# Kernel tuning notes

Hardware: AMD Instinct MI355X
Metric: run time of the kernel (lower is better)

The kernel has to match this reference:

```python
import jax, jax.numpy as jnp
import numpy as np
import math

B, N, CS, CZ = 2, 512, 384, 128
H, C, PQ, PV = 12, 16, 4, 8
EPS = 1e-8

def _quat_to_rot(q):
    q = q / jnp.linalg.norm(q, axis=-1, keepdims=True)
    a, b, c, d = q[..., 0], q[..., 1], q[..., 2], q[..., 3]
    return jnp.stack([
        jnp.stack([a*a+b*b-c*c-d*d, 2*(b*c-a*d), 2*(b*d+a*c)], -1),
        jnp.stack([2*(b*c+a*d), a*a-b*b+c*c-d*d, 2*(c*d-a*b)], -1),
        jnp.stack([2*(b*d-a*c), 2*(c*d+a*b), a*a-b*b-c*c+d*d], -1)], -2)

def setup_inputs() -> dict:
    key = jax.random.key(0)
    ks = jax.random.split(key, 12)
    def lin(k, out_f, in_f):
        return jax.random.normal(k, (out_f, in_f), jnp.float32) * math.sqrt(1.0 / in_f)
    inp = {}
    inp['single'] = jax.random.normal(ks[0], (B, N, CS), jnp.float32)
    inp['pair'] = jax.random.normal(ks[1], (B, N, N, CZ), jnp.float32)
    inp['rotations'] = _quat_to_rot(jax.random.normal(ks[2], (B, N, 4), jnp.float32))
    inp['translations'] = jax.random.normal(ks[3], (B, N, 3), jnp.float32) * 10.0
    inp['wq'] = lin(ks[4], H*C, CS); inp['bq'] = jnp.zeros((H*C,), jnp.float32)
    inp['wkv'] = lin(ks[5], 2*H*C, CS); inp['bkv'] = jnp.zeros((2*H*C,), jnp.float32)
    inp['wqp'] = lin(ks[6], 3*H*PQ, CS); inp['bqp'] = jnp.zeros((3*H*PQ,), jnp.float32)
    inp['wkvp'] = lin(ks[7], 3*H*(PQ+PV), CS); inp['bkvp'] = jnp.zeros((3*H*(PQ+PV),), jnp.float32)
    inp['wb'] = lin(ks[8], H, CZ); inp['bb'] = jnp.zeros((H,), jnp.float32)
    out_in = H*C + H*PV*4 + H*CZ  # scalar + (x,y,z,norm) points + pair
    inp['wo'] = lin(ks[9], CS, out_in); inp['bo'] = jnp.zeros((CS,), jnp.float32)
    inp['head_weights'] = jax.random.normal(ks[10], (H,), jnp.float32) * 0.1
    return inp

def _ipa(single, pair, rotations, translations, wq, bq, wkv, bkv, wqp, bqp, wkvp, bkvp, wb, bb, wo, bo, head_weights):
    b_, n_ = single.shape[0], single.shape[1]
    # scalar q/k/v
    q = (single @ wq.T + bq).reshape(b_, n_, H, C)
    kv = (single @ wkv.T + bkv).reshape(b_, n_, H, 2*C)
    k, v = kv[..., :C], kv[..., C:]
    # point q/k/v in local frames (chunk into x,y,z then stack, per _project_points)
    def proj_pts(w, bvec, P):
        raw = single @ w.T + bvec
        xc, yc, zc = jnp.split(raw, 3, axis=-1)
        return jnp.stack([xc, yc, zc], -1).reshape(b_, n_, H, P, 3)
    q_pts = proj_pts(wqp, bqp, PQ)
    kv_pts = proj_pts(wkvp, bkvp, PQ + PV)
    k_pts, v_pts = kv_pts[..., :PQ, :], kv_pts[..., PQ:, :]
    # apply rigid frames: global = R @ p + t
    def to_global(p):
        return jnp.einsum('biop,bihqp->bihqo', rotations, p) + translations[:, :, None, None, :]
    qg, kg, vg = to_global(q_pts), to_global(k_pts), to_global(v_pts)
    # scalar logits + pair bias
    bias = pair @ wb.T + bb  # [B,N,N,H]
    logits = jnp.einsum('bihc,bjhc->bhij', q, k) * math.sqrt(1.0 / (3.0 * C))
    logits = logits + math.sqrt(1.0 / 3.0) * bias.transpose(0, 3, 1, 2)
    # point-distance logits
    d2 = jnp.sum((qg[:, :, None] - kg[:, None]) ** 2, axis=-1)  # [B,N,N,H,PQ]
    gamma = jax.nn.softplus(head_weights)  # [H]
    wpt = math.sqrt(1.0 / (3.0 * PQ * 4.5))
    pt_logits = -0.5 * wpt * jnp.sum(d2, axis=-1) * gamma  # [B,N,N,H]
    attn = jax.nn.softmax(logits + pt_logits.transpose(0, 3, 1, 2), axis=-1)  # [B,H,N,N]
    # assemble output features
    out_scalar = jnp.einsum('bhij,bjhc->bihc', attn, v).reshape(b_, n_, H*C)
    rp_g = jnp.einsum('bhij,bjhpc->bihpc', attn, vg)
    # back to local frame: R^T @ (p - t)
    rp_l = jnp.einsum('bipo,bihqp->bihqo', rotations, rp_g - translations[:, :, None, None, :])
    norms = jnp.sqrt(jnp.sum(rp_l ** 2, -1) + EPS).reshape(b_, n_, H*PV)
    rp_l = rp_l.reshape(b_, n_, H*PV, 3)
    out_pair = jnp.einsum('bhij,bijd->bihd', attn, pair).reshape(b_, n_, H*CZ)
    feats = jnp.concatenate([out_scalar, rp_l[..., 0], rp_l[..., 1], rp_l[..., 2], norms, out_pair], -1)
    return feats @ wo.T + bo

def reference(single, pair, rotations, translations, wq, bq, wkv, bkv, wqp, bqp, wkvp, bkvp, wb, bb, wo, bo, head_weights):
    return _ipa(single, pair, rotations, translations, wq, bq, wkv, bkv, wqp, bqp, wkvp, bkvp, wb, bb, wo, bo, head_weights)
```

## Files before the change

### kernel.cpp

```cpp
#include <hip/hip_runtime.h>
#include <hip/hip_bf16.h>
#include <math.h>

#define NB 2
#define NN 512
#define CSD 384
#define CZD 128
#define NH 12
#define NC 16
#define NPQ 4
#define NPV 8
#define HC 192
#define QPDIM 144
#define FEATD 2112
#define WPT 0.13608276348795434f
#define RS3C 0.14433756729740643f
#define RS3 0.5773502691896258f

typedef __attribute__((ext_vector_type(8))) short short8;
typedef __attribute__((ext_vector_type(4))) float f32x4;

static __device__ inline unsigned short f2bf(float x) {
    __hip_bfloat16 h = __float2bfloat16(x);
    return *reinterpret_cast<unsigned short*>(&h);
}
static __device__ inline unsigned short bflo(float x) {
    __hip_bfloat16 h = __float2bfloat16(x);
    return f2bf(x - __bfloat162float(h));
}

#define R_S0 393216
#define R_S1 (R_S0 + 73728)
#define R_S2 (R_S1 + 147456)
#define R_S3 (R_S2 + 55296)
#define R_S4 (R_S3 + 165888)
#define R_S5 (R_S4 + 811008)
#define R_S6 (R_S5 + 2048)
__global__ __launch_bounds__(256) void k_cvt(
    const float* __restrict__ single, const float* __restrict__ wq,
    const float* __restrict__ wkv, const float* __restrict__ wqp,
    const float* __restrict__ wkvp, const float* __restrict__ wo,
    const float* __restrict__ wb,
    unsigned short* __restrict__ singleb, unsigned short* __restrict__ wallb,
    unsigned short* __restrict__ wob, unsigned short* __restrict__ wbb)
{
    int gid = blockIdx.x * 256 + threadIdx.x;
    int e = gid * 4;
    if (e >= R_S6) return;
    if (e >= R_S5) {
        int c = e - R_S5;
        int hh = c >> 7;
        ushort4 o;
        if (hh < 12) {
            float4 v = *(const float4*)(wb + hh * 128 + (c & 127));
            o.x = f2bf(v.x); o.y = f2bf(v.y); o.z = f2bf(v.z); o.w = f2bf(v.w);
        } else { o.x = 0; o.y = 0; o.z = 0; o.w = 0; }
        *(ushort4*)(wbb + c) = o;
        return;
    }
    const float* src; unsigned short* dst;
    if (e < R_S0)      { src = single + e;          dst = singleb + e; }
    else if (e < R_S1) { src = wq + (e - R_S0);     dst = wallb + (e - R_S0); }
    else if (e < R_S2) { src = wkv + (e - R_S1);    dst = wallb + 73728 + (e - R_S1); }
    else if (e < R_S3) { src = wqp + (e - R_S2);    dst = wallb + 221184 + (e - R_S2); }
    else if (e < R_S4) { src = wkvp + (e - R_S3);   dst = wallb + 276480 + (e - R_S3); }
    else               { src = wo + (e - R_S4);     dst = wob + (e - R_S4); }
    float4 v = *(const float4*)src;
    ushort4 o;
    o.x = f2bf(v.x); o.y = f2bf(v.y); o.z = f2bf(v.z); o.w = f2bf(v.w);
    *(ushort4*)dst = o;
}

__global__ __launch_bounds__(256) void k_gemm1(
    const unsigned short* __restrict__ A, const unsigned short* __restrict__ Bm,
    float* __restrict__ Cr)
{
    int w = threadIdx.x >> 6, lane = threadIdx.x & 63;
    int rt = blockIdx.x;
    int ct = blockIdx.y * 4 + w;
    int r = lane & 15, kq = lane >> 4;
    const unsigned short* ap = A  + (size_t)(rt * 16 + r) * 384 + kq * 8;
    const unsigned short* bp = Bm + (size_t)(ct * 16 + r) * 384 + kq * 8;
    f32x4 acc = {0.f, 0.f, 0.f, 0.f};
    #pragma unroll 4
    for (int ks = 0; ks < 12; ++ks) {
        short8 av = *(const short8*)(ap + ks * 32);
        short8 bv = *(const short8*)(bp + ks * 32);
        acc = __builtin_amdgcn_mfma_f32_16x16x32_bf16(av, bv, acc, 0, 0, 0);
    }
    int crow = rt * 16 + kq * 4;
    int ccol = ct * 16 + r;
    #pragma unroll
    for (int i = 0; i < 4; ++i)
        Cr[(size_t)(crow + i) * 1152 + ccol] = acc[i];
}

__global__ __launch_bounds__(256) void k_post(
    const float* __restrict__ praw, const float* __restrict__ rot, const float* __restrict__ trans,
    const float* __restrict__ hw,
    const float* __restrict__ bq, const float* __restrict__ bkv,
    const float* __restrict__ bqp, const float* __restrict__ bkvp,
    unsigned short* __restrict__ vallT2,
    unsigned short* __restrict__ qhat, unsigned short* __restrict__ khat,
    float* __restrict__ qn2, float* __restrict__ kn2)
{
    __shared__ float s_q[192], s_k[192], s_v[192], s_qp[QPDIM], s_kvp[432];
    __shared__ float s_qg[144], s_kg[144], s_vg[288];
    __shared__ float s_sh[12];
    const int t = threadIdx.x;
    const int row = blockIdx.x;
    const int b = row >> 9;
    const int i = row & 511;

    if (t < 12) {
        float sp = log1pf(expf(hw[t]));
        s_sh[t] = RS3C / (WPT * sp);
    }
    const float* pr = praw + (size_t)row * 1152;
    for (int idx = t; idx < 1152; idx += 256) {
        float v = pr[idx];
        if (idx < 192) {
            s_q[idx] = v + bq[idx];
        } else if (idx < 576) {
            int f = idx - 192; float x = v + bkv[f];
            int h = f >> 5, cc = f & 31;
            if (cc < 16) s_k[h * 16 + cc] = x;
            else         s_v[h * 16 + cc - 16] = x;
        } else if (idx < 720) {
            int f = idx - 576; s_qp[f] = v + bqp[f];
        } else {
            int f = idx - 720; s_kvp[f] = v + bkvp[f];
        }
    }
    __syncthreads();

    if (t < 192) {
        const float* R = rot + (size_t)row * 9;
        const float* T = trans + (size_t)row * 3;
        float lx, ly, lz; float* dst;
        if (t < 48) {
            lx = s_qp[t]; ly = s_qp[48 + t]; lz = s_qp[96 + t];
            dst = s_qg + t * 3;
        } else if (t < 96) {
            int idx = t - 48; int fb = (idx >> 2) * 12 + (idx & 3);
            lx = s_kvp[fb]; ly = s_kvp[144 + fb]; lz = s_kvp[288 + fb];
            dst = s_kg + idx * 3;
        } else {
            int idx = t - 96; int fb = (idx >> 3) * 12 + 4 + (idx & 7);
            lx = s_kvp[fb]; ly = s_kvp[144 + fb]; lz = s_kvp[288 + fb];
            dst = s_vg + idx * 3;
        }
        dst[0] = R[0] * lx + R[1] * ly + R[2] * lz + T[0];
        dst[1] = R[3] * lx + R[4] * ly + R[5] * lz + T[1];
        dst[2] = R[6] * lx + R[7] * ly + R[8] * lz + T[2];
    }
    __syncthreads();

    if (t < 24) {
        int h = t % 12;
        const float* g = (t < 12) ? (s_qg + h * 12) : (s_kg + h * 12);
        float s = 0.f;
        #pragma unroll
        for (int e = 0; e < 12; ++e) s += g[e] * g[e];
        float* dst = (t < 12) ? qn2 : kn2;
        dst[((size_t)b * 12 + h) * 512 + i] = s;
    }

    for (int c = t; c < 768; c += 256) {
        int h = c >> 6, cp = c & 63;
        unsigned short v;
        if (cp < 16)      v = f2bf(s_v[h * 16 + cp]);
        else if (cp < 40) v = f2bf(s_vg[h * 24 + cp - 16]);
        else              v = bflo(s_vg[h * 24 + cp - 40]);
        vallT2[((size_t)(b * 12 + h) * 64 + cp) * 512 + i] = v;
    }

    for (int idx = t; idx < 768; idx += 256) {
        int side = idx >= 384;
        int li = side ? (idx - 384) : idx;
        int h = li >> 5, s2 = li & 31;
        unsigned short o[2];
        #pragma unroll
        for (int u = 0; u < 2; ++u) {
            int k = 2 * s2 + u;
            unsigned short val = 0;
            if (!side) {
                if (k < 16)      val = f2bf(s_sh[h] * s_q[h * 16 + k]);
                else if (k < 28) val = f2bf(s_qg[h * 12 + k - 16]);
                else if (k < 40) val = f2bf(s_qg[h * 12 + k - 28]);
                else if (k < 52) val = bflo(s_qg[h * 12 + k - 40]);
            } else {
                if (k < 16)      val = f2bf(s_k[h * 16 + k]);
                else if (k < 28) val = f2bf(s_kg[h * 12 + k - 16]);
                else if (k < 40) val = bflo(s_kg[h * 12 + k - 28]);
                else if (k < 52) val = f2bf(s_kg[h * 12 + k - 40]);
            }
            o[u] = val;
        }
        unsigned short* dst = (side ? khat : qhat) + (((size_t)b * 12 + h) * 512 + i) * 64 + 2 * s2;
        *(ushort2*)dst = make_ushort2(o[0], o[1]);
    }
}

__global__ __launch_bounds__(256) void k_qk(
    const unsigned short* __restrict__ qhat, const unsigned short* __restrict__ khat,
    const float* __restrict__ qn2, const float* __restrict__ kn2,
    const float* __restrict__ hw, float* __restrict__ plog)
{
    int w = threadIdx.x >> 6, lane = threadIdx.x & 63;
    int bh = blockIdx.x;
    int i0 = (blockIdx.y >> 3) * 64;
    int j0 = (blockIdx.y & 7) * 64;
    int r = lane & 15, kq = lane >> 4;
    float sp = log1pf(expf(hw[bh % 12]));
    float m = WPT * sp;
    float coef = -0.5f * m;

    const unsigned short* ap = qhat + ((size_t)bh * 512 + i0 + w * 16 + r) * 64 + kq * 8;
    short8 a0 = *(const short8*)(ap);
    short8 a1 = *(const short8*)(ap + 32);
    const unsigned short* bpb = khat + ((size_t)bh * 512 + j0 + r) * 64 + kq * 8;
    f32x4 acc[4];
    #pragma unroll
    for (int jt = 0; jt < 4; ++jt) {
        short8 b0 = *(const short8*)(bpb + (size_t)jt * 1024);
        short8 b1 = *(const short8*)(bpb + (size_t)jt * 1024 + 32);
        f32x4 a = {0.f, 0.f, 0.f, 0.f};
        a = __builtin_amdgcn_mfma_f32_16x16x32_bf16(a0, b0, a, 0, 0, 0);
        a = __builtin_amdgcn_mfma_f32_16x16x32_bf16(a1, b1, a, 0, 0, 0);
        acc[jt] = a;
    }
    int crow = i0 + w * 16 + kq * 4;
    const float* qn = qn2 + (size_t)bh * 512;
    const float* kn = kn2 + (size_t)bh * 512;
    #pragma unroll
    for (int jt = 0; jt < 4; ++jt) {
        int ccol = j0 + jt * 16 + r;
        float knv = kn[ccol];
        #pragma unroll
        for (int ii = 0; ii < 4; ++ii)
            plog[((size_t)bh * 512 + crow + ii) * 512 + ccol] =
                m * acc[jt][ii] + coef * (qn[crow + ii] + knv);
    }
}

__global__ __launch_bounds__(512) void k_av(
    const float* __restrict__ pair,
    const unsigned short* __restrict__ wbb, const float* __restrict__ bb,
    const float* __restrict__ plog,
    unsigned short* __restrict__ attnb, unsigned short* __restrict__ featsb)
{
    __shared__ float attn12[12][521];

    const int t = threadIdx.x;
    const int row_i = blockIdx.x;
    const int b = row_i >> 9;
    const int i_loc = row_i & 511;
    const int w = t >> 6, lane = t & 63;
    const int r = lane & 15, kq = lane >> 4;

    {
        const unsigned short* bp = wbb + r * 128 + kq * 8;
        short8 bfrag[4];
        #pragma unroll
        for (int ks = 0; ks < 4; ++ks) bfrag[ks] = *(const short8*)(bp + ks * 32);
        float bbv = (r < 12) ? bb[r] : 0.f;
        #pragma unroll
        for (int tt = 0; tt < 4; ++tt) {
            int tile = w + tt * 8;
            const float* ap = pair + ((size_t)row_i * NN + tile * 16 + r) * CZD + kq * 8;
            float4 p[8];
            #pragma unroll
            for (int ks = 0; ks < 4; ++ks) {
                p[2 * ks]     = *(const float4*)(ap + ks * 32);
                p[2 * ks + 1] = *(const float4*)(ap + ks * 32 + 4);
            }
            f32x4 acc = {0.f, 0.f, 0.f, 0.f};
            #pragma unroll
            for (int ks = 0; ks < 4; ++ks) {
                short8 av;
                av[0] = (short)f2bf(p[2*ks].x);   av[1] = (short)f2bf(p[2*ks].y);
                av[2] = (short)f2bf(p[2*ks].z);   av[3] = (short)f2bf(p[2*ks].w);
                av[4] = (short)f2bf(p[2*ks+1].x); av[5] = (short)f2bf(p[2*ks+1].y);
                av[6] = (short)f2bf(p[2*ks+1].z); av[7] = (short)f2bf(p[2*ks+1].w);
                acc = __builtin_amdgcn_mfma_f32_16x16x32_bf16(av, bfrag[ks], acc, 0, 0, 0);
            }
            if (r < 12) {
                #pragma unroll
                for (int ii = 0; ii < 4; ++ii)
                    attn12[r][tile * 16 + kq * 4 + ii] = RS3 * (acc[ii] + bbv);
            }
        }
    }
    __syncthreads();

    #pragma unroll
    for (int it = 0; it < 3; ++it) {
        int idx4 = it * 512 + t;
        int h = idx4 >> 7;
        int j4 = (idx4 & 127) * 4;
        const float* lp = plog + (((size_t)b * 12 + h) * 512 + i_loc) * 512 + j4;
        float4 lv = *(const float4*)lp;
        attn12[h][j4 + 0] += lv.x;
        attn12[h][j4 + 1] += lv.y;
        attn12[h][j4 + 2] += lv.z;
        attn12[h][j4 + 3] += lv.w;
    }
    __syncthreads();

    for (int hh = w; hh < 12; hh += 8) {
        float vreg[8];
        float mx = -1e30f;
        #pragma unroll
        for (int s = 0; s < 8; ++s) { vreg[s] = attn12[hh][lane + 64 * s]; mx = fmaxf(mx, vreg[s]); }
        #pragma unroll
        for (int off = 32; off >= 1; off >>= 1) mx = fmaxf(mx, __shfl_xor(mx, off, 64));
        float ssum = 0.f;
        #pragma unroll
        for (int s = 0; s < 8; ++s) { vreg[s] = __expf(vreg[s] - mx); ssum += vreg[s]; }
        #pragma unroll
        for (int off = 32; off >= 1; off >>= 1) ssum += __shfl_xor(ssum, off, 64);
        float inv = 1.0f / ssum;
        #pragma unroll
        for (int s = 0; s < 8; ++s) attn12[hh][lane + 64 * s] = vreg[s] * inv;
    }
    __syncthreads();

    for (int idx = t; idx < 768; idx += 512) {
        int h = idx >> 6, jc = idx & 63;
        ushort4 o0, o1;
        o0.x = f2bf(attn12[h][jc * 8 + 0]); o0.y = f2bf(attn12[h][jc * 8 + 1]);
        o0.z = f2bf(attn12[h][jc * 8 + 2]); o0.w = f2bf(attn12[h][jc * 8 + 3]);
        o1.x = f2bf(attn12[h][jc * 8 + 4]); o1.y = f2bf(attn12[h][jc * 8 + 5]);
        o1.z = f2bf(attn12[h][jc * 8 + 6]); o1.w = f2bf(attn12[h][jc * 8 + 7]);
        unsigned short* gp = attnb + (((size_t)(b * 12 + h) * 512 + i_loc)) * 512 + jc * 8;
        *(ushort4*)gp = o0;
        *(ushort4*)(gp + 4) = o1;
    }
    __syncthreads();

    {
        const int d0 = w * 16;
        const int hr = (r < 12) ? r : 11;
        const unsigned short* arow = attnb + (((size_t)(b * 12 + hr) * 512 + i_loc)) * 512 + kq * 8;
        const float* pbase = pair + (size_t)row_i * NN * CZD + d0 + r;
        f32x4 acc = {0.f, 0.f, 0.f, 0.f};
        for (int ks = 0; ks < 16; ++ks) {
            int jb = ks * 32 + kq * 8;
            float x0 = pbase[(size_t)(jb + 0) * CZD];
            float x1 = pbase[(size_t)(jb + 1) * CZD];
            float x2 = pbase[(size_t)(jb + 2) * CZD];
            float x3 = pbase[(size_t)(jb + 3) * CZD];
            float x4 = pbase[(size_t)(jb + 4) * CZD];
            float x5 = pbase[(size_t)(jb + 5) * CZD];
            float x6 = pbase[(size_t)(jb + 6) * CZD];
            float x7 = pbase[(size_t)(jb + 7) * CZD];
            short8 av = *(const short8*)(arow + ks * 32);
            short8 bv;
            bv[0] = (short)f2bf(x0); bv[1] = (short)f2bf(x1);
            bv[2] = (short)f2bf(x2); bv[3] = (short)f2bf(x3);
            bv[4] = (short)f2bf(x4); bv[5] = (short)f2bf(x5);
            bv[6] = (short)f2bf(x6); bv[7] = (short)f2bf(x7);
            acc = __builtin_amdgcn_mfma_f32_16x16x32_bf16(av, bv, acc, 0, 0, 0);
        }
        unsigned short* frow = featsb + (size_t)row_i * FEATD;
        if (kq < 3) {
            #pragma unroll
            for (int ii = 0; ii < 4; ++ii)
                frow[576 + (kq * 4 + ii) * CZD + d0 + r] = f2bf(acc[ii]);
        }
    }
}

__global__ __launch_bounds__(512) void k_avg(
    const unsigned short* __restrict__ attnb, const unsigned short* __restrict__ vallT2,
    float* __restrict__ rpg, unsigned short* __restrict__ featsb)
{
    int bh = blockIdx.x;
    int itile = blockIdx.y;
    int b = bh / 12, h = bh % 12;
    int w = threadIdx.x >> 6, lane = threadIdx.x & 63;
    int mt = w >> 2, nt = w & 3;
    int r = lane & 15, kq = lane >> 4;
    int i0 = itile * 32 + mt * 16;
    const unsigned short* ap = attnb + ((size_t)bh * 512 + i0 + r) * 512 + kq * 8;
    const unsigned short* bp = vallT2 + ((size_t)bh * 64 + nt * 16 + r) * 512 + kq * 8;
    f32x4 acc = {0.f, 0.f, 0.f, 0.f};
    #pragma unroll
    for (int ks = 0; ks < 16; ++ks) {
        short8 av = *(const short8*)(ap + ks * 32);
        short8 bv = *(const short8*)(bp + ks * 32);
        acc = __builtin_amdgcn_mfma_f32_16x16x32_bf16(av, bv, acc, 0, 0, 0);
    }
    int cp = nt * 16 + r;
    #pragma unroll
    for (int ii = 0; ii < 4; ++ii) {
        int i = i0 + kq * 4 + ii;
        size_t rowg = (size_t)b * 512 + i;
        if (nt == 0) {
            featsb[rowg * FEATD + h * 16 + r] = f2bf(acc[ii]);
        } else {
            rpg[rowg * 576 + h * 48 + (cp - 16)] = acc[ii];
        }
    }
}

__global__ __launch_bounds__(128) void k_rp(
    const float* __restrict__ rpg, const float* __restrict__ rot, const float* __restrict__ trans,
    unsigned short* __restrict__ featsb)
{
    __shared__ float rot_s[9], trans_s[3];
    int row = blockIdx.x, t = threadIdx.x;
    if (t < 9) rot_s[t] = rot[(size_t)row * 9 + t];
    if (t >= 9 && t < 12) trans_s[t - 9] = trans[(size_t)row * 3 + (t - 9)];
    __syncthreads();
    if (t < 96) {
        int h = t >> 3, p = t & 7;
        const float* rp = rpg + (size_t)row * 576 + h * 48;
        float g0 = rp[p * 3 + 0] + rp[24 + p * 3 + 0];
        float g1 = rp[p * 3 + 1] + rp[24 + p * 3 + 1];
        float g2 = rp[p * 3 + 2] + rp[24 + p * 3 + 2];
        float d0 = g0 - trans_s[0], d1 = g1 - trans_s[1], d2v = g2 - trans_s[2];
        float l0 = rot_s[0] * d0 + rot_s[3] * d1 + rot_s[6] * d2v;
        float l1 = rot_s[1] * d0 + rot_s[4] * d1 + rot_s[7] * d2v;
        float l2 = rot_s[2] * d0 + rot_s[5] * d1 + rot_s[8] * d2v;
        float nrm = sqrtf(l0 * l0 + l1 * l1 + l2 * l2 + 1e-8f);
        unsigned short* frow = featsb + (size_t)row * FEATD;
        int hp = h * 8 + p;
        frow[192 + hp] = f2bf(l0);
        frow[288 + hp] = f2bf(l1);
        frow[384 + hp] = f2bf(l2);
        frow[480 + hp] = f2bf(nrm);
    }
}

__global__ __launch_bounds__(256) void k_gemm2(
    const unsigned short* __restrict__ A, const unsigned short* __restrict__ Bm,
    const float* __restrict__ bo, float* __restrict__ out)
{
    int w = threadIdx.x >> 6, lane = threadIdx.x & 63;
    int rt = blockIdx.x;
    int ct = blockIdx.y * 4 + w;
    int r = lane & 15, kq = lane >> 4;
    const unsigned short* ap = A  + (size_t)(rt * 16 + r) * FEATD + kq * 8;
    const unsigned short* bp = Bm + (size_t)(ct * 16 + r) * FEATD + kq * 8;
    f32x4 acc = {0.f, 0.f, 0.f, 0.f};
    #pragma unroll 2
    for (int ks = 0; ks < 66; ++ks) {
        short8 av = *(const short8*)(ap + ks * 32);
        short8 bv = *(const short8*)(bp + ks * 32);
        acc = __builtin_amdgcn_mfma_f32_16x16x32_bf16(av, bv, acc, 0, 0, 0);
    }
    int crow = rt * 16 + kq * 4;
    int ccol = ct * 16 + r;
    float bv = bo[ccol];
    #pragma unroll
    for (int i = 0; i < 4; ++i)
        out[(size_t)(crow + i) * CSD + ccol] = acc[i] + bv;
}

extern "C" void kernel_launch(void* const* d_in, const int* in_sizes, int n_in,
                              void* d_out, int out_size, void* d_ws, size_t ws_size,
                              hipStream_t stream) {
    const float* single = (const float*)d_in[0];
    const float* pair   = (const float*)d_in[1];
    const float* rot    = (const float*)d_in[2];
    const float* trans  = (const float*)d_in[3];
    const float* wq     = (const float*)d_in[4];
    const float* bq     = (const float*)d_in[5];
    const float* wkv    = (const float*)d_in[6];
    const float* bkv    = (const float*)d_in[7];
    const float* wqp    = (const float*)d_in[8];
    const float* bqp    = (const float*)d_in[9];
    const float* wkvp   = (const float*)d_in[10];
    const float* bkvp   = (const float*)d_in[11];
    const float* wb     = (const float*)d_in[12];
    const float* bb     = (const float*)d_in[13];
    const float* wo     = (const float*)d_in[14];
    const float* bo     = (const float*)d_in[15];
    const float* hw     = (const float*)d_in[16];
    float* out = (float*)d_out;

    float* ws = (float*)d_ws;
    float* plog    = ws;
    float* projraw = ws;
    unsigned short* qhat = (unsigned short*)(ws + 6291456);
    unsigned short* khat = (unsigned short*)(ws + 6684672);
    float* qn2     = ws + 7077888;
    float* kn2     = ws + 7090176;
    unsigned short* featsb  = (unsigned short*)(ws + 7102464);
    unsigned short* singleb = (unsigned short*)(ws + 8183808);
    unsigned short* wallb   = (unsigned short*)(ws + 8380416);
    unsigned short* wob     = (unsigned short*)(ws + 8601600);
    unsigned short* wbb     = (unsigned short*)(ws + 9007104);
    unsigned short* vallT2  = (unsigned short*)(ws + 9008128);
    unsigned short* attnb   = (unsigned short*)(ws + 9401344);
    float* rpg     = ws + 12547072;

    hipLaunchKernelGGL(k_cvt, dim3(1610), dim3(256), 0, stream,
                       single, wq, wkv, wqp, wkvp, wo, wb, singleb, wallb, wob, wbb);
    hipLaunchKernelGGL(k_gemm1, dim3(64, 18), dim3(256), 0, stream, singleb, wallb, projraw);
    hipLaunchKernelGGL(k_post, dim3(1024), dim3(256), 0, stream,
                       projraw, rot, trans, hw, bq, bkv, bqp, bkvp,
                       vallT2, qhat, khat, qn2, kn2);
    hipLaunchKernelGGL(k_qk, dim3(24, 64), dim3(256), 0, stream,
                       qhat, khat, qn2, kn2, hw, plog);
    hipLaunchKernelGGL(k_av, dim3(1024), dim3(512), 0, stream,
                       pair, wbb, bb, plog, attnb, featsb);
    hipLaunchKernelGGL(k_avg, dim3(24, 16), dim3(512), 0, stream,
                       attnb, vallT2, rpg, featsb);
    hipLaunchKernelGGL(k_rp, dim3(1024), dim3(128), 0, stream, rpg, rot, trans, featsb);
    hipLaunchKernelGGL(k_gemm2, dim3(64, 6), dim3(256), 0, stream, featsb, wob, bo, out);
}
```

Baseline: 187.6 us.

## Stage pair tiles through LDS transpose in k_av and fuse point transform into k_avg

```diff
diff --git a/kernel.cpp b/kernel.cpp
--- a/kernel.cpp
+++ b/kernel.cpp
@@ -250,7 +250,9 @@
     const float* __restrict__ plog,
     unsigned short* __restrict__ attnb, unsigned short* __restrict__ featsb)
 {
-    __shared__ float attn12[12][521];
+    __shared__ __align__(16) unsigned char smem_raw[34816];
+    float (*attn12)[521] = (float(*)[521])smem_raw;
+    unsigned short* ldsT = (unsigned short*)smem_raw;
 
     const int t = threadIdx.x;
     const int row_i = blockIdx.x;
@@ -343,43 +345,53 @@
         const int d0 = w * 16;
         const int hr = (r < 12) ? r : 11;
         const unsigned short* arow = attnb + (((size_t)(b * 12 + hr) * 512 + i_loc)) * 512 + kq * 8;
-        const float* pbase = pair + (size_t)row_i * NN * CZD + d0 + r;
+        const int jl = t >> 2, dq = t & 3;
+        const float* srcb = pair + (size_t)row_i * NN * CZD + dq * 32;
         f32x4 acc = {0.f, 0.f, 0.f, 0.f};
-        for (int ks = 0; ks < 16; ++ks) {
-            int jb = ks * 32 + kq * 8;
-            float x0 = pbase[(size_t)(jb + 0) * CZD];
-            float x1 = pbase[(size_t)(jb + 1) * CZD];
-            float x2 = pbase[(size_t)(jb + 2) * CZD];
-            float x3 = pbase[(size_t)(jb + 3) * CZD];
-            float x4 = pbase[(size_t)(jb + 4) * CZD];
-            float x5 = pbase[(size_t)(jb + 5) * CZD];
-            float x6 = pbase[(size_t)(jb + 6) * CZD];
-            float x7 = pbase[(size_t)(jb + 7) * CZD];
-            short8 av = *(const short8*)(arow + ks * 32);
-            short8 bv;
-            bv[0] = (short)f2bf(x0); bv[1] = (short)f2bf(x1);
-            bv[2] = (short)f2bf(x2); bv[3] = (short)f2bf(x3);
-            bv[4] = (short)f2bf(x4); bv[5] = (short)f2bf(x5);
-            bv[6] = (short)f2bf(x6); bv[7] = (short)f2bf(x7);
-            acc = __builtin_amdgcn_mfma_f32_16x16x32_bf16(av, bv, acc, 0, 0, 0);
+        for (int st = 0; st < 4; ++st) {
+            const float* src = srcb + (size_t)(st * 128 + jl) * CZD;
+            float4 vv[8];
+            #pragma unroll
+            for (int u = 0; u < 8; ++u) vv[u] = *(const float4*)(src + u * 4);
+            #pragma unroll
+            for (int u = 0; u < 8; ++u) {
+                int d = dq * 32 + u * 4;
+                ldsT[(size_t)(d + 0) * 136 + jl] = f2bf(vv[u].x);
+                ldsT[(size_t)(d + 1) * 136 + jl] = f2bf(vv[u].y);
+                ldsT[(size_t)(d + 2) * 136 + jl] = f2bf(vv[u].z);
+                ldsT[(size_t)(d + 3) * 136 + jl] = f2bf(vv[u].w);
+            }
+            __syncthreads();
+            #pragma unroll
+            for (int ks = 0; ks < 4; ++ks) {
+                short8 av = *(const short8*)(arow + st * 128 + ks * 32);
+                short8 bv = *(const short8*)(ldsT + (size_t)(d0 + r) * 136 + ks * 32 + kq * 8);
+                acc = __builtin_amdgcn_mfma_f32_16x16x32_bf16(av, bv, acc, 0, 0, 0);
+            }
+            __syncthreads();
         }
         unsigned short* frow = featsb + (size_t)row_i * FEATD;
         if (kq < 3) {
             #pragma unroll
-            for (int ii = 0; ii < 4; ++ii)
-                frow[576 + (kq * 4 + ii) * CZD + d0 + r] = f2bf(acc[ii]);
+            for (int ii = 0; ii < 4; ++ii) {
+                int h = kq * 4 + ii;
+                frow[576 + h * CZD + d0 + r] = f2bf(acc[ii]);
+            }
         }
     }
 }
 
 __global__ __launch_bounds__(512) void k_avg(
     const unsigned short* __restrict__ attnb, const unsigned short* __restrict__ vallT2,
-    float* __restrict__ rpg, unsigned short* __restrict__ featsb)
-{
+    const float* __restrict__ rot, const float* __restrict__ trans,
+    unsigned short* __restrict__ featsb)
+{
+    __shared__ float rp_s[32][49];
     int bh = blockIdx.x;
     int itile = blockIdx.y;
     int b = bh / 12, h = bh % 12;
-    int w = threadIdx.x >> 6, lane = threadIdx.x & 63;
+    int t = threadIdx.x;
+    int w = t >> 6, lane = t & 63;
     int mt = w >> 2, nt = w & 3;
     int r = lane & 15, kq = lane >> 4;
     int i0 = itile * 32 + mt * 16;
@@ -395,37 +407,29 @@
     int cp = nt * 16 + r;
     #pragma unroll
     for (int ii = 0; ii < 4; ++ii) {
-        int i = i0 + kq * 4 + ii;
-        size_t rowg = (size_t)b * 512 + i;
+        int il = mt * 16 + kq * 4 + ii;
         if (nt == 0) {
+            size_t rowg = (size_t)b * 512 + itile * 32 + il;
             featsb[rowg * FEATD + h * 16 + r] = f2bf(acc[ii]);
         } else {
-            rpg[rowg * 576 + h * 48 + (cp - 16)] = acc[ii];
-        }
-    }
-}
-
-__global__ __launch_bounds__(128) void k_rp(
-    const float* __restrict__ rpg, const float* __restrict__ rot, const float* __restrict__ trans,
-    unsigned short* __restrict__ featsb)
-{
-    __shared__ float rot_s[9], trans_s[3];
-    int row = blockIdx.x, t = threadIdx.x;
-    if (t < 9) rot_s[t] = rot[(size_t)row * 9 + t];
-    if (t >= 9 && t < 12) trans_s[t - 9] = trans[(size_t)row * 3 + (t - 9)];
-    __syncthreads();
-    if (t < 96) {
-        int h = t >> 3, p = t & 7;
-        const float* rp = rpg + (size_t)row * 576 + h * 48;
-        float g0 = rp[p * 3 + 0] + rp[24 + p * 3 + 0];
-        float g1 = rp[p * 3 + 1] + rp[24 + p * 3 + 1];
-        float g2 = rp[p * 3 + 2] + rp[24 + p * 3 + 2];
-        float d0 = g0 - trans_s[0], d1 = g1 - trans_s[1], d2v = g2 - trans_s[2];
-        float l0 = rot_s[0] * d0 + rot_s[3] * d1 + rot_s[6] * d2v;
-        float l1 = rot_s[1] * d0 + rot_s[4] * d1 + rot_s[7] * d2v;
-        float l2 = rot_s[2] * d0 + rot_s[5] * d1 + rot_s[8] * d2v;
+            rp_s[il][cp - 16] = acc[ii];
+        }
+    }
+    __syncthreads();
+    if (t < 256) {
+        int il = t >> 3, p = t & 7;
+        size_t rowg = (size_t)b * 512 + itile * 32 + il;
+        const float* R = rot + rowg * 9;
+        const float* T = trans + rowg * 3;
+        float g0 = rp_s[il][p * 3 + 0] + rp_s[il][24 + p * 3 + 0];
+        float g1 = rp_s[il][p * 3 + 1] + rp_s[il][24 + p * 3 + 1];
+        float g2 = rp_s[il][p * 3 + 2] + rp_s[il][24 + p * 3 + 2];
+        float d0 = g0 - T[0], d1 = g1 - T[1], d2v = g2 - T[2];
+        float l0 = R[0] * d0 + R[3] * d1 + R[6] * d2v;
+        float l1 = R[1] * d0 + R[4] * d1 + R[7] * d2v;
+        float l2 = R[2] * d0 + R[5] * d1 + R[8] * d2v;
         float nrm = sqrtf(l0 * l0 + l1 * l1 + l2 * l2 + 1e-8f);
-        unsigned short* frow = featsb + (size_t)row * FEATD;
+        unsigned short* frow = featsb + rowg * FEATD;
         int hp = h * 8 + p;
         frow[192 + hp] = f2bf(l0);
         frow[288 + hp] = f2bf(l1);
@@ -495,7 +499,6 @@
     unsigned short* wbb     = (unsigned short*)(ws + 9007104);
     unsigned short* vallT2  = (unsigned short*)(ws + 9008128);
     unsigned short* attnb   = (unsigned short*)(ws + 9401344);
-    float* rpg     = ws + 12547072;
 
     hipLaunchKernelGGL(k_cvt, dim3(1610), dim3(256), 0, stream,
                        single, wq, wkv, wqp, wkvp, wo, wb, singleb, wallb, wob, wbb);
@@ -508,7 +511,6 @@
     hipLaunchKernelGGL(k_av, dim3(1024), dim3(512), 0, stream,
                        pair, wbb, bb, plog, attnb, featsb);
     hipLaunchKernelGGL(k_avg, dim3(24, 16), dim3(512), 0, stream,
-                       attnb, vallT2, rpg, featsb);
-    hipLaunchKernelGGL(k_rp, dim3(1024), dim3(128), 0, stream, rpg, rot, trans, featsb);
+                       attnb, vallT2, rot, trans, featsb);
     hipLaunchKernelGGL(k_gemm2, dim3(64, 6), dim3(256), 0, stream, featsb, wob, bo, out);
 }
```

After: 202.3 us. +7.8%, slower.
